# Kernel tuning notes

Hardware: AMD Instinct MI355X
Metric: run time of the kernel (lower is better)

The kernel has to match this reference:

```python
import math
import jax, jax.numpy as jnp
import numpy as np

N = 4096        # num nodes
IN_DIM = 512
H0 = 64         # hidden_dim[0]
H1 = 64         # hidden_dim[-1]
HEADS = 4
N_CLASSES = 10


def setup_inputs() -> dict:
    key = jax.random.key(0)
    ks = jax.random.split(key, 10)
    feats = jax.random.normal(ks[0], (N, IN_DIM), dtype=jnp.float32)
    counting_attn = jax.random.uniform(ks[1], (N, N), dtype=jnp.float32)
    s1 = 1.0 / math.sqrt(IN_DIM)
    s2 = 1.0 / math.sqrt(H0 * HEADS)
    # layer-1 heads, stacked: [H, out, in] (torch Linear weight layout)
    Wq1 = jax.random.normal(ks[2], (HEADS, H0, IN_DIM), dtype=jnp.float32) * s1
    Wk1 = jax.random.normal(ks[3], (HEADS, H0, IN_DIM), dtype=jnp.float32) * s1
    Wv1 = jax.random.normal(ks[4], (HEADS, H0, IN_DIM), dtype=jnp.float32) * s1
    # layer-2 single head: [out, in]
    Wq2 = jax.random.normal(ks[5], (H1, H0 * HEADS), dtype=jnp.float32) * s2
    Wk2 = jax.random.normal(ks[6], (H1, H0 * HEADS), dtype=jnp.float32) * s2
    Wv2 = jax.random.normal(ks[7], (H1, H0 * HEADS), dtype=jnp.float32) * s2
    Wc = jax.random.normal(ks[8], (N_CLASSES, H1), dtype=jnp.float32) * (1.0 / math.sqrt(H1))
    bc = jax.random.normal(ks[9], (N_CLASSES,), dtype=jnp.float32) * 0.01
    return {"feats": feats, "counting_attn": counting_attn,
            "Wq1": Wq1, "Wk1": Wk1, "Wv1": Wv1,
            "Wq2": Wq2, "Wk2": Wk2, "Wv2": Wv2,
            "Wc": Wc, "bc": bc}


def _gkat_heads(feat, Wq, Wk, Wv, counting):
    # feat: [N, in], Wq/Wk/Wv: [H, d, in], counting: [N, N] -> [N, H*d]
    Q = jnp.einsum('ni,hdi->hnd', feat, Wq)
    K = jnp.einsum('ni,hdi->hnd', feat, Wk)
    V = jnp.einsum('ni,hdi->hnd', feat, Wv)
    d = Q.shape[-1]
    logits = jnp.einsum('hnd,hmd->hnm', Q, K) / jnp.sqrt(jnp.asarray(d, Q.dtype))
    e = jnp.exp(logits - jnp.max(logits, axis=-1, keepdims=True))
    a = jnp.einsum('hnm,mk->hnk', e, counting)          # exp(logits) @ counting_attn
    a = a / (jnp.sum(a, axis=-1, keepdims=True) + 1e-9)  # row-normalize
    ret = jnp.einsum('hnm,hmd->hnd', a, V)
    ret = jax.nn.elu(ret)
    H, n, dd = ret.shape
    return jnp.transpose(ret, (1, 0, 2)).reshape(n, H * dd)  # concat heads along dim=1


def reference(feats, counting_attn, Wq1, Wk1, Wv1, Wq2, Wk2, Wv2, Wc, bc):
    # normalize over feature dim (torch.std is unbiased -> ddof=1)
    mean_ = jnp.mean(feats, axis=1, keepdims=True)
    std_ = jnp.std(feats, axis=1, keepdims=True, ddof=1)
    h = (feats - mean_) / (std_ + 1e-9)
    h = _gkat_heads(h, Wq1, Wk1, Wv1, counting_attn)                 # [N, H*H0]
    h = _gkat_heads(h, Wq2[None], Wk2[None], Wv2[None], counting_attn)  # [N, H1]
    return h @ Wc.T + bc
```

## Files before the change

kernel.cpp:

```cpp
#include <hip/hip_runtime.h>
#include <hip/hip_bf16.h>
#include <math.h>

#define NN4   4096
#define QSCALE 0.180336880111120420f

typedef __attribute__((ext_vector_type(8))) short short8;
typedef __attribute__((ext_vector_type(8))) unsigned short ushort8;
typedef __attribute__((ext_vector_type(4))) unsigned short ushort4v;
typedef __attribute__((ext_vector_type(4))) float f32x4;

__device__ __forceinline__ unsigned short f2b(float f) {
  union { __hip_bfloat16 h; unsigned short u; } v;
  v.h = __float2bfloat16(f);
  return v.u;
}
__device__ __forceinline__ float b2f(unsigned short s) {
  return __uint_as_float(((unsigned int)s) << 16);
}
__device__ __forceinline__ ushort8 cvt8(f32x4 a, f32x4 b) {
  return (ushort8){f2b(a[0]), f2b(a[1]), f2b(a[2]), f2b(a[3]),
                   f2b(b[0]), f2b(b[1]), f2b(b[2]), f2b(b[3])};
}

#define GLOAD16(gp, lp) __builtin_amdgcn_global_load_lds( \
    (const __attribute__((address_space(1))) void*)(gp),  \
    (__attribute__((address_space(3))) void*)(lp), 16, 0, 0)

__global__ __launch_bounds__(256) void k_norm(const float* __restrict__ x,
                                              unsigned short* __restrict__ y) {
  int row  = blockIdx.x * 4 + (threadIdx.x >> 6);
  int lane = threadIdx.x & 63;
  const float4* src = (const float4*)(x + (size_t)row * 512);
  float4 a = src[lane];
  float4 b = src[lane + 64];
  float s = a.x + a.y + a.z + a.w + b.x + b.y + b.z + b.w;
#pragma unroll
  for (int off = 32; off; off >>= 1) s += __shfl_xor(s, off);
  float mean = s * (1.0f / 512.0f);
  float ssq = 0.f, d;
  d = a.x - mean; ssq += d * d;  d = a.y - mean; ssq += d * d;
  d = a.z - mean; ssq += d * d;  d = a.w - mean; ssq += d * d;
  d = b.x - mean; ssq += d * d;  d = b.y - mean; ssq += d * d;
  d = b.z - mean; ssq += d * d;  d = b.w - mean; ssq += d * d;
#pragma unroll
  for (int off = 32; off; off >>= 1) ssq += __shfl_xor(ssq, off);
  float inv = 1.0f / (sqrtf(ssq * (1.0f / 511.0f)) + 1e-9f);
  unsigned short* dst = y + (size_t)row * 512;
  ushort4v va = (ushort4v){f2b((a.x - mean) * inv), f2b((a.y - mean) * inv),
                           f2b((a.z - mean) * inv), f2b((a.w - mean) * inv)};
  ushort4v vb = (ushort4v){f2b((b.x - mean) * inv), f2b((b.y - mean) * inv),
                           f2b((b.z - mean) * inv), f2b((b.w - mean) * inv)};
  *(ushort4v*)(dst + lane * 4)       = va;
  *(ushort4v*)(dst + 256 + lane * 4) = vb;
}

__global__ __launch_bounds__(256) void k_projqkv(
    const unsigned short* __restrict__ Ap, int K,
    const float* __restrict__ Wq, const float* __restrict__ Wk,
    const float* __restrict__ Wv, int N, int nT,
    unsigned short* __restrict__ Qo, unsigned short* __restrict__ Ko,
    unsigned short* __restrict__ VT, int padrows, float qscale) {
  __shared__ unsigned short As[128 * 40];
  __shared__ unsigned short Bs[128 * 40];
  const int tid = threadIdx.x;
  const int sel = blockIdx.y / nT;
  const int n0 = (blockIdx.y % nT) * 128;
  const int m0 = blockIdx.x * 128;
  const float* Bp = sel == 0 ? Wq : (sel == 1 ? Wk : Wv);
  const float bscale = sel == 0 ? qscale : 1.0f;
  const int lane = tid & 63, wid = tid >> 6;
  const int hi = lane >> 4, lo = lane & 15;
  const int wr = (wid >> 1) << 6, wc = (wid & 1) << 6;
  const int srow = tid >> 1, sk = (tid & 1) << 4;
  f32x4 acc[4][4];
#pragma unroll
  for (int i = 0; i < 4; ++i)
#pragma unroll
    for (int j = 0; j < 4; ++j) acc[i][j] = (f32x4){0.f, 0.f, 0.f, 0.f};

  for (int k0 = 0; k0 < K; k0 += 32) {
    ushort8 va0, va1, vb0, vb1;
    {
      const unsigned short* s = Ap + (size_t)(m0 + srow) * K + k0 + sk;
      va0 = *(const ushort8*)(s);
      va1 = *(const ushort8*)(s + 8);
    }
    {
      int gr = n0 + srow;
      if (gr < N) {
        const float* s = Bp + (size_t)gr * K + k0 + sk;
        f32x4 f0 = *(const f32x4*)(s) * bscale;
        f32x4 f1 = *(const f32x4*)(s + 4) * bscale;
        f32x4 f2 = *(const f32x4*)(s + 8) * bscale;
        f32x4 f3 = *(const f32x4*)(s + 12) * bscale;
        vb0 = cvt8(f0, f1); vb1 = cvt8(f2, f3);
      } else { vb0 = (ushort8)0; vb1 = (ushort8)0; }
    }
    __syncthreads();
    *(ushort8*)&As[srow * 40 + sk]     = va0;
    *(ushort8*)&As[srow * 40 + sk + 8] = va1;
    *(ushort8*)&Bs[srow * 40 + sk]     = vb0;
    *(ushort8*)&Bs[srow * 40 + sk + 8] = vb1;
    __syncthreads();
    short8 af[4], bf[4];
#pragma unroll
    for (int i = 0; i < 4; ++i)
      af[i] = *(const short8*)&As[(wr + (i << 4) + lo) * 40 + hi * 8];
#pragma unroll
    for (int j = 0; j < 4; ++j)
      bf[j] = *(const short8*)&Bs[(wc + (j << 4) + lo) * 40 + hi * 8];
#pragma unroll
    for (int i = 0; i < 4; ++i)
#pragma unroll
      for (int j = 0; j < 4; ++j)
        acc[i][j] = __builtin_amdgcn_mfma_f32_16x16x32_bf16(af[i], bf[j], acc[i][j], 0, 0, 0);
  }

  if (sel < 2) {
    unsigned short* Cp = sel == 0 ? Qo : Ko;
#pragma unroll
    for (int i = 0; i < 4; ++i)
#pragma unroll
      for (int j = 0; j < 4; ++j)
#pragma unroll
        for (int reg = 0; reg < 4; ++reg) {
          int r = m0 + wr + (i << 4) + (hi << 2) + reg;
          int c = n0 + wc + (j << 4) + lo;
          if (c < N) Cp[(size_t)r * N + c] = f2b(acc[i][j][reg]);
        }
  } else {
#pragma unroll
    for (int i = 0; i < 4; ++i)
#pragma unroll
      for (int j = 0; j < 4; ++j) {
        int c = n0 + wc + (j << 4) + lo;
        if (c < N) {
          int hh = c >> 6, dd = c & 63;
          int rb = m0 + wr + (i << 4) + (hi << 2);
          ushort4v pk = (ushort4v){f2b(acc[i][j][0]), f2b(acc[i][j][1]),
                                   f2b(acc[i][j][2]), f2b(acc[i][j][3])};
          *(ushort4v*)&VT[(size_t)(hh * 68 + dd) * NN4 + rb] = pk;
        }
      }
    int hstart = n0 >> 6;
    int hcnt = (N - n0) >> 6; if (hcnt > 2) hcnt = 2;
    int tot = hcnt * padrows * 128;
    for (int e = tid; e < tot; e += 256) {
      int hh = hstart + e / (padrows * 128);
      int rem = e % (padrows * 128);
      int j = rem >> 7, col = m0 + (rem & 127);
      VT[(size_t)(hh * 68 + 64 + j) * NN4 + col] = (j == 0) ? 0x3F80 : 0;
    }
  }
}

template<int NF>
__global__ __launch_bounds__(256, 3) void k_cvxg(
    const float* __restrict__ cnt,
    const unsigned short* __restrict__ Bt,
    unsigned short* __restrict__ Pb) {
  constexpr int LDB = NF * 16;
  __shared__ unsigned short As[2][64 * 40];
  __shared__ unsigned short Bs[2][LDB * 32];
  const int tid = threadIdx.x, lane = tid & 63, wid = tid >> 6;
  const int hi = lane >> 4, lo = lane & 15;
  const int m0 = blockIdx.x * 64;
  const int kbeg = blockIdx.y << 8, kend = kbeg + 256;
  const int arow = tid >> 2, ak = (tid & 3) << 3;
  const int boff = (lo * 64 + hi * 16) ^ (((lo >> 1) & 3) << 4);

  f32x4 acc[NF];
#pragma unroll
  for (int j = 0; j < NF; ++j) acc[j] = (f32x4){0.f, 0.f, 0.f, 0.f};

  f32x4 ar0, ar1;
  {
    const float* s = cnt + (size_t)(m0 + arow) * 4096 + kbeg + ak;
    ar0 = *(const f32x4*)(s); ar1 = *(const f32x4*)(s + 4);
  }
  for (int c = wid; c < NF; c += 4) {
    int P = c * 1024 + lane * 16;
    int L = P ^ ((P >> 3) & 0x30);
    GLOAD16(Bt + (size_t)(L >> 6) * 4096 + kbeg + ((L & 63) >> 1),
            (char*)&Bs[0][0] + c * 1024);
  }
  *(ushort8*)&As[0][arow * 40 + ak] = cvt8(ar0, ar1);
  asm volatile("s_waitcnt vmcnt(0)" ::: "memory");
  __syncthreads();

  for (int k0 = kbeg; k0 < kend; k0 += 32) {
    const int cur = ((k0 - kbeg) >> 5) & 1, nxt = cur ^ 1;
    const bool more = (k0 + 32 < kend);
    if (more) {
      const float* s = cnt + (size_t)(m0 + arow) * 4096 + (k0 + 32) + ak;
      ar0 = *(const f32x4*)(s); ar1 = *(const f32x4*)(s + 4);
      for (int c = wid; c < NF; c += 4) {
        int P = c * 1024 + lane * 16;
        int L = P ^ ((P >> 3) & 0x30);
        GLOAD16(Bt + (size_t)(L >> 6) * 4096 + (k0 + 32) + ((L & 63) >> 1),
                (char*)&Bs[nxt][0] + c * 1024);
      }
    }
    short8 af0 = *(const short8*)&As[cur][(16 * wid + lo) * 40 + hi * 8];
    __builtin_amdgcn_s_setprio(1);
#pragma unroll
    for (int j = 0; j < NF; ++j) {
      short8 bf = *(const short8*)((const char*)&Bs[cur][0] + j * 1024 + boff);
      acc[j] = __builtin_amdgcn_mfma_f32_16x16x32_bf16(af0, bf, acc[j], 0, 0, 0);
    }
    __builtin_amdgcn_s_setprio(0);
    if (more) *(ushort8*)&As[nxt][arow * 40 + ak] = cvt8(ar0, ar1);
    asm volatile("s_waitcnt vmcnt(0)" ::: "memory");
    __syncthreads();
  }
  unsigned short* P = Pb + (size_t)blockIdx.y * 4096 * LDB;
#pragma unroll
  for (int j = 0; j < NF; ++j)
#pragma unroll
    for (int reg = 0; reg < 4; ++reg) {
      int r = m0 + 16 * wid + 4 * hi + reg;
      P[(size_t)r * LDB + 16 * j + lo] = f2b(acc[j][reg]);
    }
}

__global__ __launch_bounds__(256) void k_tredB(const unsigned short* __restrict__ in, int ld,
                                               int nsl, unsigned short* __restrict__ out,
                                               int orow) {
  __shared__ float t[64][65];
  const int n0 = blockIdx.x << 6, d0 = blockIdx.y << 6;
  const int o  = threadIdx.x & 7;
  const int rr = threadIdx.x >> 3;
  const size_t pstride = (size_t)4096 * ld;
  const bool valid = (o * 8) < (ld - d0);
#pragma unroll
  for (int pass = 0; pass < 2; ++pass) {
    const int r = rr + (pass << 5);
    float a[8] = {0.f, 0.f, 0.f, 0.f, 0.f, 0.f, 0.f, 0.f};
    if (valid) {
      const unsigned short* p = in + (size_t)(n0 + r) * ld + d0 + o * 8;
      for (int z = 0; z < nsl; ++z) {
        ushort8 v = *(const ushort8*)(p + (size_t)z * pstride);
#pragma unroll
        for (int k = 0; k < 8; ++k) a[k] += b2f(v[k]);
      }
    }
#pragma unroll
    for (int k = 0; k < 8; ++k) t[o * 8 + k][r] = a[k];
  }
  __syncthreads();
  const int c = threadIdx.x & 63, r4 = threadIdx.x >> 6;
#pragma unroll
  for (int i = 0; i < 16; ++i) {
    int dr = r4 + (i << 2);
    if (d0 + dr < orow)
      out[(size_t)(d0 + dr) * 4096 + n0 + c] = f2b(t[dr][c]);
  }
}

__global__ __launch_bounds__(256, 2) void k_attn(
    const unsigned short* __restrict__ Qg, const unsigned short* __restrict__ Kg,
    int ldqk, const unsigned short* __restrict__ CVg,
    unsigned short* __restrict__ Pb) {
  __shared__ unsigned short Ks[128 * 72];
  __shared__ unsigned short Cs[80 * 136];
  __shared__ unsigned short Es[128 * 136];
  const int tid = threadIdx.x, lane = tid & 63, wid = tid >> 6;
  const int hi = lane >> 4, lo = lane & 15;
  const int qb = blockIdx.x, h = blockIdx.y, sl = blockIdx.z;
  const int n0 = qb * 128;
  const int MS = 4096 / gridDim.z;
  const int m0beg = sl * MS;
  const int wr = (wid >> 1) << 6, wc = (wid & 1) << 6;

  short8 qf[4][2];
  const unsigned short* Qh = Qg + (size_t)h * 64;
#pragma unroll
  for (int j = 0; j < 4; ++j)
#pragma unroll
    for (int t = 0; t < 2; ++t)
      qf[j][t] = *(const short8*)(Qh + (size_t)(n0 + wc + 16 * j + lo) * ldqk + t * 32 + hi * 8);

  const unsigned short* CVh = CVg + (size_t)h * 68 * NN4;
  const unsigned short* Kh  = Kg + (size_t)h * 64;

  const int krow = tid >> 1, khalf = (tid & 1) << 5;
  int crdR[5], crdW[5], ccol[5];
#pragma unroll
  for (int k = 0; k < 5; ++k) {
    int c = tid + k * 256;
    int row = c >> 4;
    crdW[k] = row;
    crdR[k] = row < 68 ? row : 67;
    ccol[k] = (c & 15) << 3;
  }
  ushort8 krg[4], crg[5];

  auto LOADK = [&](int m0) {
    const unsigned short* src = Kh + (size_t)(m0 + krow) * ldqk + khalf;
    krg[0] = *(const ushort8*)(src);
    krg[1] = *(const ushort8*)(src + 8);
    krg[2] = *(const ushort8*)(src + 16);
    krg[3] = *(const ushort8*)(src + 24);
  };
  auto LOADC = [&](int m0) {
#pragma unroll
    for (int k = 0; k < 5; ++k)
      crg[k] = *(const ushort8*)(CVh + (size_t)crdR[k] * NN4 + m0 + ccol[k]);
  };
  auto WRITEK = [&]() {
    unsigned short* dp = &Ks[krow * 72 + khalf];
    *(ushort8*)(dp) = krg[0];      *(ushort8*)(dp + 8) = krg[1];
    *(ushort8*)(dp + 16) = krg[2]; *(ushort8*)(dp + 24) = krg[3];
  };
  auto WRITEC = [&]() {
#pragma unroll
    for (int k = 0; k < 5; ++k)
      *(ushort8*)&Cs[crdW[k] * 136 + ccol[k]] = crg[k];
  };

  f32x4 accn[2][5];
#pragma unroll
  for (int i = 0; i < 2; ++i)
#pragma unroll
    for (int j = 0; j < 5; ++j) accn[i][j] = (f32x4){0.f, 0.f, 0.f, 0.f};

  LOADK(m0beg); LOADC(m0beg);
  WRITEK(); WRITEC();
  __syncthreads();

  for (int mt = 0; mt < MS; mt += 128) {
    const int m0 = m0beg + mt;
    const bool more = (mt + 128) < MS;
    if (more) { LOADK(m0 + 128); LOADC(m0 + 128); }
    short8 kf[4][2];
#pragma unroll
    for (int i = 0; i < 4; ++i)
#pragma unroll
      for (int t = 0; t < 2; ++t)
        kf[i][t] = *(const short8*)&Ks[(wr + 16 * i + lo) * 72 + t * 32 + hi * 8];
    f32x4 s[4][4];
#pragma unroll
    for (int i = 0; i < 4; ++i)
#pragma unroll
      for (int j = 0; j < 4; ++j) s[i][j] = (f32x4){0.f, 0.f, 0.f, 0.f};
    __builtin_amdgcn_s_setprio(1);
#pragma unroll
    for (int t = 0; t < 2; ++t)
#pragma unroll
      for (int i = 0; i < 4; ++i)
#pragma unroll
        for (int j = 0; j < 4; ++j)
          s[i][j] = __builtin_amdgcn_mfma_f32_16x16x32_bf16(kf[i][t], qf[j][t], s[i][j], 0, 0, 0);
    __builtin_amdgcn_s_setprio(0);
#pragma unroll
    for (int i = 0; i < 4; ++i)
#pragma unroll
      for (int j = 0; j < 4; ++j) {
        unsigned int u0 = (unsigned int)f2b(__builtin_amdgcn_exp2f(s[i][j][0])) |
                          ((unsigned int)f2b(__builtin_amdgcn_exp2f(s[i][j][1])) << 16);
        unsigned int u1 = (unsigned int)f2b(__builtin_amdgcn_exp2f(s[i][j][2])) |
                          ((unsigned int)f2b(__builtin_amdgcn_exp2f(s[i][j][3])) << 16);
        unsigned long long pk = (unsigned long long)u0 | ((unsigned long long)u1 << 32);
        int row = wc + 16 * j + lo;
        int byte = row * 272 + (wr + 16 * i + 4 * hi) * 2;
        *(unsigned long long*)((char*)Es + (byte ^ ((row & 7) << 5))) = pk;
      }
    __syncthreads();
    if (more) WRITEK();
    __builtin_amdgcn_s_setprio(1);
#pragma unroll
    for (int t2 = 0; t2 < 4; ++t2) {
      int r0 = 32 * wid + lo, r1 = r0 + 16;
      int cb = (t2 * 32 + hi * 8) * 2;
      short8 ea0 = *(const short8*)((const char*)Es + ((r0 * 272 + cb) ^ ((r0 & 7) << 5)));
      short8 ea1 = *(const short8*)((const char*)Es + ((r1 * 272 + cb) ^ ((r1 & 7) << 5)));
      short8 cbv[5];
#pragma unroll
      for (int j2 = 0; j2 < 5; ++j2)
        cbv[j2] = *(const short8*)&Cs[(16 * j2 + lo) * 136 + t2 * 32 + hi * 8];
#pragma unroll
      for (int j2 = 0; j2 < 5; ++j2) {
        accn[0][j2] = __builtin_amdgcn_mfma_f32_16x16x32_bf16(ea0, cbv[j2], accn[0][j2], 0, 0, 0);
        accn[1][j2] = __builtin_amdgcn_mfma_f32_16x16x32_bf16(ea1, cbv[j2], accn[1][j2], 0, 0, 0);
      }
    }
    __builtin_amdgcn_s_setprio(0);
    __syncthreads();
    if (more) { WRITEC(); __syncthreads(); }
  }
  unsigned short* P = Pb + (((size_t)h * gridDim.x + qb) * gridDim.z + sl) * (128 * 80);
#pragma unroll
  for (int i2 = 0; i2 < 2; ++i2)
#pragma unroll
    for (int j2 = 0; j2 < 5; ++j2)
#pragma unroll
      for (int reg = 0; reg < 4; ++reg) {
        int r = 32 * wid + 16 * i2 + 4 * hi + reg;
        int c = 16 * j2 + lo;
        P[(size_t)r * 80 + c] = f2b(accn[i2][j2][reg]);
      }
}

__global__ void k_fin2(const unsigned short* __restrict__ parts, int nsl,
                       unsigned short* __restrict__ hb, int ldh) {
  int idx = blockIdx.x * 256 + threadIdx.x;
  int d = idx & 63, r = (idx >> 6) & 4095, h = idx >> 18;
  size_t b0 = ((size_t)(h * 32 + (r >> 7)) * nsl) * 10240 + (size_t)(r & 127) * 80;
  float nm = 0.f, dn = 0.f;
  for (int sl = 0; sl < nsl; ++sl) {
    const unsigned short* p = parts + b0 + (size_t)sl * 10240;
    nm += b2f(p[d]); dn += b2f(p[64]);
  }
  float x = nm / (dn + 1e-9f);
  x = x > 0.f ? x : expm1f(x);
  hb[(size_t)r * ldh + h * 64 + d] = f2b(x);
}

__global__ __launch_bounds__(256) void k_fincls(const unsigned short* __restrict__ parts,
                                                int nsl, const float* __restrict__ Wc,
                                                const float* __restrict__ bc,
                                                float* __restrict__ out) {
  int r = blockIdx.x * 4 + (threadIdx.x >> 6);
  int d = threadIdx.x & 63;
  size_t b0 = ((size_t)(r >> 7) * nsl) * 10240 + (size_t)(r & 127) * 80;
  float nm = 0.f, dn = 0.f;
  for (int sl = 0; sl < nsl; ++sl) {
    const unsigned short* p = parts + b0 + (size_t)sl * 10240;
    nm += b2f(p[d]); dn += b2f(p[64]);
  }
  float x = nm / (dn + 1e-9f);
  x = x > 0.f ? x : expm1f(x);
#pragma unroll
  for (int cl = 0; cl < 10; ++cl) {
    float v = x * Wc[cl * 64 + d];
#pragma unroll
    for (int off = 32; off; off >>= 1) v += __shfl_xor(v, off);
    if (d == 0) out[(size_t)r * 10 + cl] = v + bc[cl];
  }
}

extern "C" void kernel_launch(void* const* d_in, const int* in_sizes, int n_in,
                              void* d_out, int out_size, void* d_ws, size_t ws_size,
                              hipStream_t stream) {
  (void)in_sizes; (void)n_in; (void)out_size; (void)ws_size;
  const float* feats    = (const float*)d_in[0];
  const float* counting = (const float*)d_in[1];
  const float* Wq1 = (const float*)d_in[2];
  const float* Wk1 = (const float*)d_in[3];
  const float* Wv1 = (const float*)d_in[4];
  const float* Wq2 = (const float*)d_in[5];
  const float* Wk2 = (const float*)d_in[6];
  const float* Wv2 = (const float*)d_in[7];
  const float* Wc  = (const float*)d_in[8];
  const float* bc  = (const float*)d_in[9];
  float* out = (float*)d_out;

  char* w = (char*)d_ws;
  size_t off = 0;
  auto alloc = [&](size_t bytes) { void* p = w + off; off += (bytes + 255) & ~(size_t)255; return p; };
  unsigned short* hnb    = (unsigned short*)alloc((size_t)4096 * 512 * 2);
  unsigned short* Q1b    = (unsigned short*)alloc((size_t)4096 * 256 * 2);
  unsigned short* K1b    = (unsigned short*)alloc((size_t)4096 * 256 * 2);
  unsigned short* V1xT   = (unsigned short*)alloc((size_t)272 * 4096 * 2);
  unsigned short* CVX1Tb = (unsigned short*)alloc((size_t)272 * 4096 * 2);
  unsigned short* h1b    = (unsigned short*)alloc((size_t)4096 * 256 * 2);
  unsigned short* Q2b    = (unsigned short*)alloc((size_t)4096 * 64 * 2);
  unsigned short* K2b    = (unsigned short*)alloc((size_t)4096 * 64 * 2);
  unsigned short* V2xT   = (unsigned short*)alloc((size_t)80 * 4096 * 2);
  unsigned short* CVX2Tb = (unsigned short*)alloc((size_t)68 * 4096 * 2);
  unsigned short* big    = (unsigned short*)alloc((size_t)36 * 1024 * 1024);

  k_norm<<<1024, 256, 0, stream>>>(feats, hnb);

  k_projqkv<<<dim3(32, 6), 256, 0, stream>>>(hnb, 512, Wq1, Wk1, Wv1, 256, 2,
                                             Q1b, K1b, V1xT, 4, QSCALE);
  k_cvxg<17><<<dim3(64, 16), 256, 0, stream>>>(counting, V1xT, big);
  k_tredB<<<dim3(64, 5), 256, 0, stream>>>(big, 272, 16, CVX1Tb, 272);
  k_attn<<<dim3(32, 4, 4), 256, 0, stream>>>(Q1b, K1b, 256, CVX1Tb, big);
  k_fin2<<<4096, 256, 0, stream>>>(big, 4, h1b, 256);

  k_projqkv<<<dim3(32, 3), 256, 0, stream>>>(h1b, 256, Wq2, Wk2, Wv2, 64, 1,
                                             Q2b, K2b, V2xT, 16, QSCALE);
  k_cvxg<5><<<dim3(64, 16), 256, 0, stream>>>(counting, V2xT, big);
  k_tredB<<<dim3(64, 2), 256, 0, stream>>>(big, 80, 16, CVX2Tb, 68);
  k_attn<<<dim3(32, 1, 16), 256, 0, stream>>>(Q2b, K2b, 64, CVX2Tb, big);
  k_fincls<<<1024, 256, 0, stream>>>(big, 16, Wc, bc, out);
}
```

Before: 167.6 us.

## Pre-convert counting matrix to bf16 once and double cvxg row tile

Adds a kernel that converts the 4096x4096 fp32 counting matrix to bf16 once, so both counting-times-V GEMMs read half the bytes and can load A tiles straight into swizzled LDS with direct global-to-LDS loads instead of converting in registers. The cvxg kernel now covers 128 rows per block with two MFMA accumulator sets per wave, reusing each B fragment twice and halving the grid. The cost is an extra full pass over the 64MB fp32 matrix plus a 32MB bf16 write, and more registers per thread, which may limit occupancy.

```diff
diff --git a/kernel.cpp b/kernel.cpp
--- a/kernel.cpp
+++ b/kernel.cpp
@@ -53,6 +53,17 @@
                            f2b((b.z - mean) * inv), f2b((b.w - mean) * inv)};
   *(ushort4v*)(dst + lane * 4)       = va;
   *(ushort4v*)(dst + 256 + lane * 4) = vb;
+}
+
+__global__ __launch_bounds__(256) void k_cvtcnt(const float* __restrict__ in,
+                                                unsigned short* __restrict__ out) {
+  size_t i = ((size_t)blockIdx.x * 256 + threadIdx.x) * 8;
+  const size_t stride = (size_t)gridDim.x * 256 * 8;
+  for (; i < (size_t)4096 * 4096; i += stride) {
+    f32x4 a = *(const f32x4*)(in + i);
+    f32x4 b = *(const f32x4*)(in + i + 4);
+    *(ushort8*)(out + i) = cvt8(a, b);
+  }
 }
 
 __global__ __launch_bounds__(256) void k_projqkv(
@@ -155,73 +166,76 @@
   }
 }
 
-template<int NF>
-__global__ __launch_bounds__(256, 3) void k_cvxg(
-    const float* __restrict__ cnt,
+template<int NF, int MINW>
+__global__ __launch_bounds__(256, MINW) void k_cvxg(
+    const unsigned short* __restrict__ cntB,
     const unsigned short* __restrict__ Bt,
     unsigned short* __restrict__ Pb) {
   constexpr int LDB = NF * 16;
-  __shared__ unsigned short As[2][64 * 40];
-  __shared__ unsigned short Bs[2][LDB * 32];
+  __shared__ unsigned short As[2][4096];
+  __shared__ unsigned short Bs[2][NF * 512];
   const int tid = threadIdx.x, lane = tid & 63, wid = tid >> 6;
   const int hi = lane >> 4, lo = lane & 15;
-  const int m0 = blockIdx.x * 64;
+  const int m0 = blockIdx.x * 128;
   const int kbeg = blockIdx.y << 8, kend = kbeg + 256;
-  const int arow = tid >> 2, ak = (tid & 3) << 3;
   const int boff = (lo * 64 + hi * 16) ^ (((lo >> 1) & 3) << 4);
 
-  f32x4 acc[NF];
-#pragma unroll
-  for (int j = 0; j < NF; ++j) acc[j] = (f32x4){0.f, 0.f, 0.f, 0.f};
-
-  f32x4 ar0, ar1;
-  {
-    const float* s = cnt + (size_t)(m0 + arow) * 4096 + kbeg + ak;
-    ar0 = *(const f32x4*)(s); ar1 = *(const f32x4*)(s + 4);
-  }
-  for (int c = wid; c < NF; c += 4) {
-    int P = c * 1024 + lane * 16;
-    int L = P ^ ((P >> 3) & 0x30);
-    GLOAD16(Bt + (size_t)(L >> 6) * 4096 + kbeg + ((L & 63) >> 1),
-            (char*)&Bs[0][0] + c * 1024);
-  }
-  *(ushort8*)&As[0][arow * 40 + ak] = cvt8(ar0, ar1);
+  f32x4 acc[2][NF];
+#pragma unroll
+  for (int i = 0; i < 2; ++i)
+#pragma unroll
+    for (int j = 0; j < NF; ++j) acc[i][j] = (f32x4){0.f, 0.f, 0.f, 0.f};
+
+  auto STAGE = [&](int k0, int buf) {
+#pragma unroll
+    for (int s = 0; s < 2; ++s) {
+      int ch = s * 4 + wid;
+      int row = ch * 16 + (lane >> 2);
+      int hia = (lane & 3) ^ ((row >> 1) & 3);
+      GLOAD16(cntB + (size_t)(m0 + row) * 4096 + k0 + hia * 8,
+              (char*)&As[buf][0] + ch * 1024);
+    }
+    for (int c = wid; c < NF; c += 4) {
+      int P = c * 1024 + lane * 16;
+      int L = P ^ ((P >> 3) & 0x30);
+      GLOAD16(Bt + (size_t)(L >> 6) * 4096 + k0 + ((L & 63) >> 1),
+              (char*)&Bs[buf][0] + c * 1024);
+    }
+  };
+
+  STAGE(kbeg, 0);
   asm volatile("s_waitcnt vmcnt(0)" ::: "memory");
   __syncthreads();
 
+  const int r0 = 32 * wid + lo, r1 = r0 + 16;
+  const int ho = ((hi ^ ((r0 >> 1) & 3)) << 3);
+
   for (int k0 = kbeg; k0 < kend; k0 += 32) {
     const int cur = ((k0 - kbeg) >> 5) & 1, nxt = cur ^ 1;
-    const bool more = (k0 + 32 < kend);
-    if (more) {
-      const float* s = cnt + (size_t)(m0 + arow) * 4096 + (k0 + 32) + ak;
-      ar0 = *(const f32x4*)(s); ar1 = *(const f32x4*)(s + 4);
-      for (int c = wid; c < NF; c += 4) {
-        int P = c * 1024 + lane * 16;
-        int L = P ^ ((P >> 3) & 0x30);
-        GLOAD16(Bt + (size_t)(L >> 6) * 4096 + (k0 + 32) + ((L & 63) >> 1),
-                (char*)&Bs[nxt][0] + c * 1024);
-      }
-    }
-    short8 af0 = *(const short8*)&As[cur][(16 * wid + lo) * 40 + hi * 8];
+    if (k0 + 32 < kend) STAGE(k0 + 32, nxt);
+    short8 af0 = *(const short8*)&As[cur][r0 * 32 + ho];
+    short8 af1 = *(const short8*)&As[cur][r1 * 32 + ho];
     __builtin_amdgcn_s_setprio(1);
 #pragma unroll
     for (int j = 0; j < NF; ++j) {
       short8 bf = *(const short8*)((const char*)&Bs[cur][0] + j * 1024 + boff);
-      acc[j] = __builtin_amdgcn_mfma_f32_16x16x32_bf16(af0, bf, acc[j], 0, 0, 0);
+      acc[0][j] = __builtin_amdgcn_mfma_f32_16x16x32_bf16(af0, bf, acc[0][j], 0, 0, 0);
+      acc[1][j] = __builtin_amdgcn_mfma_f32_16x16x32_bf16(af1, bf, acc[1][j], 0, 0, 0);
     }
     __builtin_amdgcn_s_setprio(0);
-    if (more) *(ushort8*)&As[nxt][arow * 40 + ak] = cvt8(ar0, ar1);
     asm volatile("s_waitcnt vmcnt(0)" ::: "memory");
     __syncthreads();
   }
   unsigned short* P = Pb + (size_t)blockIdx.y * 4096 * LDB;
 #pragma unroll
-  for (int j = 0; j < NF; ++j)
-#pragma unroll
-    for (int reg = 0; reg < 4; ++reg) {
-      int r = m0 + 16 * wid + 4 * hi + reg;
-      P[(size_t)r * LDB + 16 * j + lo] = f2b(acc[j][reg]);
-    }
+  for (int i = 0; i < 2; ++i)
+#pragma unroll
+    for (int j = 0; j < NF; ++j)
+#pragma unroll
+      for (int reg = 0; reg < 4; ++reg) {
+        int r = m0 + 32 * wid + 16 * i + 4 * hi + reg;
+        P[(size_t)r * LDB + 16 * j + lo] = f2b(acc[i][j][reg]);
+      }
 }
 
 __global__ __launch_bounds__(256) void k_tredB(const unsigned short* __restrict__ in, int ld,
@@ -469,20 +483,22 @@
   unsigned short* K2b    = (unsigned short*)alloc((size_t)4096 * 64 * 2);
   unsigned short* V2xT   = (unsigned short*)alloc((size_t)80 * 4096 * 2);
   unsigned short* CVX2Tb = (unsigned short*)alloc((size_t)68 * 4096 * 2);
+  unsigned short* cntB   = (unsigned short*)alloc((size_t)4096 * 4096 * 2);
   unsigned short* big    = (unsigned short*)alloc((size_t)36 * 1024 * 1024);
 
   k_norm<<<1024, 256, 0, stream>>>(feats, hnb);
+  k_cvtcnt<<<2048, 256, 0, stream>>>(counting, cntB);
 
   k_projqkv<<<dim3(32, 6), 256, 0, stream>>>(hnb, 512, Wq1, Wk1, Wv1, 256, 2,
                                              Q1b, K1b, V1xT, 4, QSCALE);
-  k_cvxg<17><<<dim3(64, 16), 256, 0, stream>>>(counting, V1xT, big);
+  k_cvxg<17, 3><<<dim3(32, 16), 256, 0, stream>>>(cntB, V1xT, big);
   k_tredB<<<dim3(64, 5), 256, 0, stream>>>(big, 272, 16, CVX1Tb, 272);
   k_attn<<<dim3(32, 4, 4), 256, 0, stream>>>(Q1b, K1b, 256, CVX1Tb, big);
   k_fin2<<<4096, 256, 0, stream>>>(big, 4, h1b, 256);
 
   k_projqkv<<<dim3(32, 3), 256, 0, stream>>>(h1b, 256, Wq2, Wk2, Wv2, 64, 1,
                                              Q2b, K2b, V2xT, 16, QSCALE);
-  k_cvxg<5><<<dim3(64, 16), 256, 0, stream>>>(counting, V2xT, big);
+  k_cvxg<5, 4><<<dim3(32, 16), 256, 0, stream>>>(cntB, V2xT, big);
   k_tredB<<<dim3(64, 2), 256, 0, stream>>>(big, 80, 16, CVX2Tb, 68);
   k_attn<<<dim3(32, 1, 16), 256, 0, stream>>>(Q2b, K2b, 64, CVX2Tb, big);
   k_fincls<<<1024, 256, 0, stream>>>(big, 16, Wc, bc, out);
```

Result: slower. 175.1 us (+4.5%).
